# Optimization experiments

Measured on AMD Instinct MI355X. Metric: run time of the kernel, lower is better.

The kernel has to match this reference:

```python
import jax, jax.numpy as jnp
import numpy as np

B, S, D, E, H, K = 2, 2048, 1024, 8, 4096, 2  # batch, seq, n_embed, num_experts, 4*n_embed, top_k


def setup_inputs() -> dict:
    key = jax.random.key(0)
    ks = jax.random.split(key, 10)
    w = lambda k, shape: (jax.random.normal(k, shape, jnp.float32) * 0.02)
    return {
        "x": jax.random.normal(ks[0], (B, S, D), jnp.float32),
        "noise": jax.random.normal(ks[1], (B, S, E), jnp.float32),  # replaces torch.randn_like
        "Wr": w(ks[2], (D, E)),  # topkroute_linear
        "br": jnp.zeros((E,), jnp.float32),
        "Wn": w(ks[3], (D, E)),  # noise_linear
        "bn": jnp.zeros((E,), jnp.float32),
        "W1": w(ks[4], (E, D, H)),  # per-expert first Linear
        "b1": jnp.zeros((E, H), jnp.float32),
        "W2": w(ks[5], (E, H, D)),  # per-expert second Linear
        "b2": jnp.zeros((E, D), jnp.float32),
    }


def reference(x, noise, Wr, br, Wn, bn, W1, b1, W2, b2):
    # --- NoisyTopkRouter ---
    logits = jnp.einsum('bsd,de->bse', x, Wr) + br
    noise_logits = jnp.einsum('bsd,de->bse', x, Wn) + bn
    noisy_logits = logits + noise * jax.nn.softplus(noise_logits)
    _, topi = jax.lax.top_k(noisy_logits, K)                      # [B,S,K]
    sel = (topi[..., :, None] == jnp.arange(E)).any(axis=-2)      # [B,S,E] bool
    gates = jax.nn.softmax(jnp.where(sel, noisy_logits, -jnp.inf), axis=-1)  # sparse softmax
    softmax_gating = jax.nn.softmax(logits, axis=-1)

    # --- expert dispatch: gate is exactly 0 for non-selected experts, so the
    # masked gather/scatter loop equals a gate-weighted sum over all experts ---
    h = jax.nn.relu(jnp.einsum('bsd,edh->ebsh', x, W1) + b1[:, None, None, :])  # [E,B,S,H]
    y = jnp.einsum('ebsh,ehd->ebsd', h, W2) + b2[:, None, None, :]              # [E,B,S,D]
    final = jnp.einsum('bse,ebsd->bsd', gates, y)
    return final, softmax_gating
```

## Files before the change

kernel.cpp:

```cpp
#include <hip/hip_runtime.h>
#include <stdint.h>

#define T_TOK 4096
#define Dm    1024
#define Em    8
#define Hm    4096
#define NSLOT (2 * T_TOK)
#define KSPLIT 2

typedef __bf16 bf16x8 __attribute__((ext_vector_type(8)));
typedef float  f32x4  __attribute__((ext_vector_type(4)));
typedef unsigned short us8v __attribute__((ext_vector_type(8)));

__device__ __forceinline__ unsigned short f2bf(float f) {
  union { float f; unsigned int u; } c; c.f = f;
  unsigned int u = c.u;
  unsigned int r = u + 0x7fffu + ((u >> 16) & 1u);
  return (unsigned short)(r >> 16);
}

__device__ __forceinline__ void async16(const void* g, void* l) {
  __builtin_amdgcn_global_load_lds(
      (const __attribute__((address_space(1))) void*)g,
      (__attribute__((address_space(3))) void*)l, 16, 0, 0);
}

__global__ __launch_bounds__(256) void transpose_cvt_kernel(
    const float* __restrict__ src, unsigned short* __restrict__ dst, int R, int C) {
  __shared__ float tile[128][33];
  const int e = blockIdx.z;
  const float* s = src + (size_t)e * R * C;
  unsigned short* d = dst + (size_t)e * R * C;
  const int c0 = blockIdx.x * 32, r0 = blockIdx.y * 128;
  const int tid = threadIdx.x;

  const int lrow = tid >> 3, lc = (tid & 7) * 4;
#pragma unroll
  for (int p = 0; p < 4; ++p) {
    const int row = lrow + p * 32;
    float4 v = *(const float4*)(s + (size_t)(r0 + row) * C + c0 + lc);
    tile[row][lc + 0] = v.x; tile[row][lc + 1] = v.y;
    tile[row][lc + 2] = v.z; tile[row][lc + 3] = v.w;
  }
  __syncthreads();

  const int rb = (tid & 15) * 8;
#pragma unroll
  for (int p = 0; p < 2; ++p) {
    const int c = (tid >> 4) + p * 16;
    us8v o;
#pragma unroll
    for (int k = 0; k < 8; ++k) o[k] = f2bf(tile[rb + k][c]);
    *(us8v*)(d + (size_t)(c0 + c) * R + r0 + rb) = o;
  }
}

__global__ __launch_bounds__(256) void router_kernel(
    const float* __restrict__ x, const float* __restrict__ noise,
    const float* __restrict__ Wr, const float* __restrict__ br,
    const float* __restrict__ Wn, const float* __restrict__ bn,
    float* __restrict__ out_gating, int* __restrict__ lists,
    int* __restrict__ counts, float* __restrict__ gslot,
    unsigned short* __restrict__ xbf) {
  const int wave = threadIdx.x >> 6, lane = threadIdx.x & 63;
  const int t = blockIdx.x * 4 + wave;
  const float* xt = x + (size_t)t * Dm;
  float accR[Em] = {}, accN[Em] = {};
  for (int d = lane; d < Dm; d += 64) {
    const float xv = xt[d];
    xbf[(size_t)t * Dm + d] = f2bf(xv);
    const float* wr = Wr + d * Em;
    const float* wn = Wn + d * Em;
#pragma unroll
    for (int e = 0; e < Em; e++) { accR[e] += xv * wr[e]; accN[e] += xv * wn[e]; }
  }
#pragma unroll
  for (int e = 0; e < Em; e++)
    for (int off = 32; off > 0; off >>= 1) {
      accR[e] += __shfl_down(accR[e], off, 64);
      accN[e] += __shfl_down(accN[e], off, 64);
    }
  if (lane == 0) {
    float lg[Em], ny[Em];
#pragma unroll
    for (int e = 0; e < Em; e++) {
      lg[e] = accR[e] + br[e];
      float nl = accN[e] + bn[e];
      float sp = fmaxf(nl, 0.f) + log1pf(expf(-fabsf(nl)));
      ny[e] = lg[e] + noise[(size_t)t * Em + e] * sp;
    }
    int i0 = 0;
#pragma unroll
    for (int e = 1; e < Em; e++) if (ny[e] > ny[i0]) i0 = e;
    int i1 = (i0 == 0) ? 1 : 0;
#pragma unroll
    for (int e = 0; e < Em; e++) if (e != i0 && ny[e] > ny[i1]) i1 = e;
    const float e1 = expf(ny[i1] - ny[i0]);
    const float g0 = 1.f / (1.f + e1), g1 = e1 / (1.f + e1);
    float m = lg[0];
#pragma unroll
    for (int e = 1; e < Em; e++) m = fmaxf(m, lg[e]);
    float s = 0.f;
#pragma unroll
    for (int e = 0; e < Em; e++) s += expf(lg[e] - m);
#pragma unroll
    for (int e = 0; e < Em; e++) out_gating[(size_t)t * Em + e] = expf(lg[e] - m) / s;
    int p0 = atomicAdd(&counts[i0], 1); lists[i0 * T_TOK + p0] = t;
    int p1 = atomicAdd(&counts[i1], 1); lists[i1 * T_TOK + p1] = t;
    gslot[i0 * T_TOK + p0] = g0;
    gslot[i1 * T_TOK + p1] = g1;
  }
}

__global__ __launch_bounds__(256) void gemm1_kernel(
    const unsigned short* __restrict__ xbf, const unsigned short* __restrict__ w1bf,
    const float* __restrict__ b1, const int* __restrict__ counts,
    const int* __restrict__ lists, unsigned short* __restrict__ hbuf) {
  const int e = blockIdx.x;
  const int cnt = counts[e];
  const int m0 = blockIdx.y * 128;
  if (m0 >= cnt) return;
  const int n0 = blockIdx.z * 128;
  int base = 0;
  for (int i = 0; i < e; i++) base += counts[i];

  __shared__ __align__(16) unsigned short As[3][128 * 32];
  __shared__ __align__(16) unsigned short Bs[3][128 * 32];
  __shared__ int tok[128];

  const int tid = threadIdx.x;
  if (tid < 128) {
    int m = m0 + tid;
    tok[tid] = (m < cnt) ? lists[e * T_TOK + m] : 0;
  }
  __syncthreads();

  const int part = tid & 3;
  const int r0 = tid >> 2;
  const int r1 = r0 + 64;
  const size_t gA0 = (size_t)tok[r0] * Dm + part * 8;
  const size_t gA1 = (size_t)tok[r1] * Dm + part * 8;
  const size_t gB0 = ((size_t)e * Hm + n0 + r0) * Dm + part * 8;
  const size_t gB1 = ((size_t)e * Hm + n0 + r1) * Dm + part * 8;

  const int lane = tid & 63, wv = tid >> 6;
  const int quad = lane >> 4, l15 = lane & 15;
  const int wm = (wv >> 1) * 64, wn = (wv & 1) * 64;
  const int lds_off = wv * 512;

  f32x4 acc[4][4] = {};

  async16(xbf + gA0,       As[0] + lds_off);
  async16(xbf + gA1,       As[0] + 2048 + lds_off);
  async16(w1bf + gB0,      Bs[0] + lds_off);
  async16(w1bf + gB1,      Bs[0] + 2048 + lds_off);
  async16(xbf + gA0 + 32,  As[1] + lds_off);
  async16(xbf + gA1 + 32,  As[1] + 2048 + lds_off);
  async16(w1bf + gB0 + 32, Bs[1] + lds_off);
  async16(w1bf + gB1 + 32, Bs[1] + 2048 + lds_off);

  const int NI = Dm / 32;
  int cur = 0;
  for (int it = 0; it < NI; ++it) {
    if (it < NI - 1) {
      asm volatile("s_waitcnt vmcnt(4)" ::: "memory");
    } else {
      asm volatile("s_waitcnt vmcnt(0)" ::: "memory");
    }
    __builtin_amdgcn_s_barrier();
    __builtin_amdgcn_sched_barrier(0);
    if (it + 2 < NI) {
      const int k0 = (it + 2) * 32;
      int nb = cur + 2; if (nb >= 3) nb -= 3;
      async16(xbf + gA0 + k0, As[nb] + lds_off);
      async16(xbf + gA1 + k0, As[nb] + 2048 + lds_off);
      async16(w1bf + gB0 + k0, Bs[nb] + lds_off);
      async16(w1bf + gB1 + k0, Bs[nb] + 2048 + lds_off);
    }
    bf16x8 af[4], bfv[4];
#pragma unroll
    for (int i = 0; i < 4; i++)
      af[i] = *(const bf16x8*)(As[cur] + (wm + i * 16 + l15) * 32 + quad * 8);
#pragma unroll
    for (int j = 0; j < 4; j++)
      bfv[j] = *(const bf16x8*)(Bs[cur] + (wn + j * 16 + l15) * 32 + quad * 8);
#pragma unroll
    for (int i = 0; i < 4; i++)
#pragma unroll
      for (int j = 0; j < 4; j++)
        acc[i][j] = __builtin_amdgcn_mfma_f32_16x16x32_bf16(af[i], bfv[j], acc[i][j], 0, 0, 0);
    cur = (cur == 2) ? 0 : cur + 1;
  }

#pragma unroll
  for (int i = 0; i < 4; i++)
#pragma unroll
    for (int r = 0; r < 4; r++) {
      const int ml = wm + i * 16 + quad * 4 + r;
      const int m = m0 + ml;
      if (m < cnt) {
#pragma unroll
        for (int j = 0; j < 4; j++) {
          const int n = n0 + wn + j * 16 + l15;
          float v = acc[i][j][r] + b1[(size_t)e * Hm + n];
          v = fmaxf(v, 0.f);
          hbuf[(size_t)(base + m) * Hm + n] = f2bf(v);
        }
      }
    }
}

__global__ __launch_bounds__(256) void gemm2_kernel(
    const unsigned short* __restrict__ hbuf, const unsigned short* __restrict__ w2bf,
    const int* __restrict__ counts, const int* __restrict__ lists,
    const float* __restrict__ gslot, const float* __restrict__ b2,
    float* __restrict__ out) {
  const int e = blockIdx.x;
  const int ks = blockIdx.z & 1;
  const int cnt = counts[e];
  const int m0 = blockIdx.y * 128;
  if (m0 >= cnt) return;
  const int n0 = (blockIdx.z >> 1) * 128;
  int base = 0;
  for (int i = 0; i < e; i++) base += counts[i];
  const int kbase = ks * (Hm / KSPLIT);

  __shared__ __align__(16) unsigned short As[3][128 * 32];
  __shared__ __align__(16) unsigned short Bs[3][128 * 32];
  __shared__ int tok[128];
  __shared__ float gt[128];

  const int tid = threadIdx.x;
  if (tid < 128) {
    int m = m0 + tid;
    tok[tid] = (m < cnt) ? lists[e * T_TOK + m] : 0;
    gt[tid]  = (m < cnt) ? gslot[e * T_TOK + m] : 0.f;
  }
  __syncthreads();

  const int part = tid & 3;
  const int r0 = tid >> 2;
  const int r1 = r0 + 64;
  const int rowA0 = min(base + m0 + r0, NSLOT - 1);
  const int rowA1 = min(base + m0 + r1, NSLOT - 1);
  const size_t gA0 = (size_t)rowA0 * Hm + kbase + part * 8;
  const size_t gA1 = (size_t)rowA1 * Hm + kbase + part * 8;
  const size_t gB0 = ((size_t)e * Dm + n0 + r0) * Hm + kbase + part * 8;
  const size_t gB1 = ((size_t)e * Dm + n0 + r1) * Hm + kbase + part * 8;

  const int lane = tid & 63, wv = tid >> 6;
  const int quad = lane >> 4, l15 = lane & 15;
  const int wm = (wv >> 1) * 64, wn = (wv & 1) * 64;
  const int lds_off = wv * 512;

  f32x4 acc[4][4] = {};

  async16(hbuf + gA0,       As[0] + lds_off);
  async16(hbuf + gA1,       As[0] + 2048 + lds_off);
  async16(w2bf + gB0,       Bs[0] + lds_off);
  async16(w2bf + gB1,       Bs[0] + 2048 + lds_off);
  async16(hbuf + gA0 + 32,  As[1] + lds_off);
  async16(hbuf + gA1 + 32,  As[1] + 2048 + lds_off);
  async16(w2bf + gB0 + 32,  Bs[1] + lds_off);
  async16(w2bf + gB1 + 32,  Bs[1] + 2048 + lds_off);

  const int NI = Hm / KSPLIT / 32;
  int cur = 0;
  for (int it = 0; it < NI; ++it) {
    if (it < NI - 1) {
      asm volatile("s_waitcnt vmcnt(4)" ::: "memory");
    } else {
      asm volatile("s_waitcnt vmcnt(0)" ::: "memory");
    }
    __builtin_amdgcn_s_barrier();
    __builtin_amdgcn_sched_barrier(0);
    if (it + 2 < NI) {
      const int k0 = (it + 2) * 32;
      int nb = cur + 2; if (nb >= 3) nb -= 3;
      async16(hbuf + gA0 + k0, As[nb] + lds_off);
      async16(hbuf + gA1 + k0, As[nb] + 2048 + lds_off);
      async16(w2bf + gB0 + k0, Bs[nb] + lds_off);
      async16(w2bf + gB1 + k0, Bs[nb] + 2048 + lds_off);
    }
    bf16x8 af[4], bfv[4];
#pragma unroll
    for (int i = 0; i < 4; i++)
      af[i] = *(const bf16x8*)(As[cur] + (wm + i * 16 + l15) * 32 + quad * 8);
#pragma unroll
    for (int j = 0; j < 4; j++)
      bfv[j] = *(const bf16x8*)(Bs[cur] + (wn + j * 16 + l15) * 32 + quad * 8);
#pragma unroll
    for (int i = 0; i < 4; i++)
#pragma unroll
      for (int j = 0; j < 4; j++)
        acc[i][j] = __builtin_amdgcn_mfma_f32_16x16x32_bf16(af[i], bfv[j], acc[i][j], 0, 0, 0);
    cur = (cur == 2) ? 0 : cur + 1;
  }

#pragma unroll
  for (int i = 0; i < 4; i++)
#pragma unroll
    for (int r = 0; r < 4; r++) {
      const int ml = wm + i * 16 + quad * 4 + r;
      const int m = m0 + ml;
      if (m < cnt) {
        const int t = tok[ml];
        const float g = gt[ml];
        float* orow = out + (size_t)t * Dm + n0;
#pragma unroll
        for (int j = 0; j < 4; j++) {
          const int n = wn + j * 16 + l15;
          float v = acc[i][j][r];
          if (ks == 0) v += b2[(size_t)e * Dm + n0 + n];
          atomicAdd(orow + n, g * v);
        }
      }
    }
}

extern "C" void kernel_launch(void* const* d_in, const int* in_sizes, int n_in,
                              void* d_out, int out_size, void* d_ws, size_t ws_size,
                              hipStream_t stream) {
  const float* x     = (const float*)d_in[0];
  const float* noise = (const float*)d_in[1];
  const float* Wr    = (const float*)d_in[2];
  const float* br    = (const float*)d_in[3];
  const float* Wn    = (const float*)d_in[4];
  const float* bn    = (const float*)d_in[5];
  const float* W1    = (const float*)d_in[6];
  const float* b1    = (const float*)d_in[7];
  const float* W2    = (const float*)d_in[8];
  const float* b2    = (const float*)d_in[9];

  float* out        = (float*)d_out;
  float* out_gating = out + (size_t)T_TOK * Dm;

  char* ws = (char*)d_ws;
  unsigned short* w1bf = (unsigned short*)(ws);
  unsigned short* w2bf = (unsigned short*)(ws + 67108864);
  unsigned short* xbf  = (unsigned short*)(ws + 134217728);
  unsigned short* hbuf = (unsigned short*)(ws + 142606336);
  int*   lists         = (int*)(ws + 209715200);
  float* gslot         = (float*)(ws + 209846272);
  int*   counts        = (int*)(ws + 209977344);

  hipMemsetAsync(counts, 0, Em * sizeof(int), stream);
  hipMemsetAsync(out, 0, (size_t)T_TOK * Dm * sizeof(float), stream);

  transpose_cvt_kernel<<<dim3(Hm / 32, Dm / 128, Em), 256, 0, stream>>>(W1, w1bf, Dm, Hm);
  transpose_cvt_kernel<<<dim3(Dm / 32, Hm / 128, Em), 256, 0, stream>>>(W2, w2bf, Hm, Dm);

  router_kernel<<<T_TOK / 4, 256, 0, stream>>>(x, noise, Wr, br, Wn, bn,
                                               out_gating, lists, counts, gslot, xbf);

  gemm1_kernel<<<dim3(Em, 16, Hm / 128), 256, 0, stream>>>(xbf, w1bf, b1, counts, lists, hbuf);
  gemm2_kernel<<<dim3(Em, 16, (Dm / 128) * KSPLIT), 256, 0, stream>>>(hbuf, w2bf, counts, lists,
                                                                      gslot, b2, out);
}
```

Before: 753.9 us.

## Use 256x128 tiles with 512 threads and replace atomic scatter with combine kernel

```diff
diff --git a/kernel.cpp b/kernel.cpp
--- a/kernel.cpp
+++ b/kernel.cpp
@@ -6,7 +6,6 @@
 #define Em    8
 #define Hm    4096
 #define NSLOT (2 * T_TOK)
-#define KSPLIT 2
 
 typedef __bf16 bf16x8 __attribute__((ext_vector_type(8)));
 typedef float  f32x4  __attribute__((ext_vector_type(4)));
@@ -60,7 +59,8 @@
     const float* __restrict__ Wr, const float* __restrict__ br,
     const float* __restrict__ Wn, const float* __restrict__ bn,
     float* __restrict__ out_gating, int* __restrict__ lists,
-    int* __restrict__ counts, float* __restrict__ gslot,
+    int* __restrict__ counts, int* __restrict__ expt,
+    int* __restrict__ pos, float* __restrict__ gsel,
     unsigned short* __restrict__ xbf) {
   const int wave = threadIdx.x >> 6, lane = threadIdx.x & 63;
   const int t = blockIdx.x * 4 + wave;
@@ -107,41 +107,40 @@
     for (int e = 0; e < Em; e++) out_gating[(size_t)t * Em + e] = expf(lg[e] - m) / s;
     int p0 = atomicAdd(&counts[i0], 1); lists[i0 * T_TOK + p0] = t;
     int p1 = atomicAdd(&counts[i1], 1); lists[i1 * T_TOK + p1] = t;
-    gslot[i0 * T_TOK + p0] = g0;
-    gslot[i1 * T_TOK + p1] = g1;
-  }
-}
-
-__global__ __launch_bounds__(256) void gemm1_kernel(
+    expt[2 * t] = i0; expt[2 * t + 1] = i1;
+    pos[2 * t] = p0;  pos[2 * t + 1] = p1;
+    gsel[2 * t] = g0; gsel[2 * t + 1] = g1;
+  }
+}
+
+__global__ __launch_bounds__(512) void gemm1_kernel(
     const unsigned short* __restrict__ xbf, const unsigned short* __restrict__ w1bf,
     const float* __restrict__ b1, const int* __restrict__ counts,
     const int* __restrict__ lists, unsigned short* __restrict__ hbuf) {
   const int e = blockIdx.x;
   const int cnt = counts[e];
-  const int m0 = blockIdx.y * 128;
+  const int m0 = blockIdx.y * 256;
   if (m0 >= cnt) return;
   const int n0 = blockIdx.z * 128;
   int base = 0;
   for (int i = 0; i < e; i++) base += counts[i];
 
-  __shared__ __align__(16) unsigned short As[3][128 * 32];
+  __shared__ __align__(16) unsigned short As[3][256 * 32];
   __shared__ __align__(16) unsigned short Bs[3][128 * 32];
-  __shared__ int tok[128];
+  __shared__ int tok[256];
 
   const int tid = threadIdx.x;
-  if (tid < 128) {
+  if (tid < 256) {
     int m = m0 + tid;
     tok[tid] = (m < cnt) ? lists[e * T_TOK + m] : 0;
   }
   __syncthreads();
 
   const int part = tid & 3;
-  const int r0 = tid >> 2;
-  const int r1 = r0 + 64;
-  const size_t gA0 = (size_t)tok[r0] * Dm + part * 8;
-  const size_t gA1 = (size_t)tok[r1] * Dm + part * 8;
-  const size_t gB0 = ((size_t)e * Hm + n0 + r0) * Dm + part * 8;
-  const size_t gB1 = ((size_t)e * Hm + n0 + r1) * Dm + part * 8;
+  const int rr = tid >> 2;
+  const size_t gA0 = (size_t)tok[rr] * Dm + part * 8;
+  const size_t gA1 = (size_t)tok[rr + 128] * Dm + part * 8;
+  const size_t gB0 = ((size_t)e * Hm + n0 + rr) * Dm + part * 8;
 
   const int lane = tid & 63, wv = tid >> 6;
   const int quad = lane >> 4, l15 = lane & 15;
@@ -151,19 +150,17 @@
   f32x4 acc[4][4] = {};
 
   async16(xbf + gA0,       As[0] + lds_off);
-  async16(xbf + gA1,       As[0] + 2048 + lds_off);
+  async16(xbf + gA1,       As[0] + 4096 + lds_off);
   async16(w1bf + gB0,      Bs[0] + lds_off);
-  async16(w1bf + gB1,      Bs[0] + 2048 + lds_off);
   async16(xbf + gA0 + 32,  As[1] + lds_off);
-  async16(xbf + gA1 + 32,  As[1] + 2048 + lds_off);
+  async16(xbf + gA1 + 32,  As[1] + 4096 + lds_off);
   async16(w1bf + gB0 + 32, Bs[1] + lds_off);
-  async16(w1bf + gB1 + 32, Bs[1] + 2048 + lds_off);
 
   const int NI = Dm / 32;
   int cur = 0;
   for (int it = 0; it < NI; ++it) {
     if (it < NI - 1) {
-      asm volatile("s_waitcnt vmcnt(4)" ::: "memory");
+      asm volatile("s_waitcnt vmcnt(3)" ::: "memory");
     } else {
       asm volatile("s_waitcnt vmcnt(0)" ::: "memory");
     }
@@ -173,9 +170,8 @@
       const int k0 = (it + 2) * 32;
       int nb = cur + 2; if (nb >= 3) nb -= 3;
       async16(xbf + gA0 + k0, As[nb] + lds_off);
-      async16(xbf + gA1 + k0, As[nb] + 2048 + lds_off);
+      async16(xbf + gA1 + k0, As[nb] + 4096 + lds_off);
       async16(w1bf + gB0 + k0, Bs[nb] + lds_off);
-      async16(w1bf + gB1 + k0, Bs[nb] + 2048 + lds_off);
     }
     bf16x8 af[4], bfv[4];
 #pragma unroll
@@ -210,43 +206,28 @@
     }
 }
 
-__global__ __launch_bounds__(256) void gemm2_kernel(
+__global__ __launch_bounds__(512) void gemm2_kernel(
     const unsigned short* __restrict__ hbuf, const unsigned short* __restrict__ w2bf,
-    const int* __restrict__ counts, const int* __restrict__ lists,
-    const float* __restrict__ gslot, const float* __restrict__ b2,
-    float* __restrict__ out) {
+    const int* __restrict__ counts, float* __restrict__ ybuf) {
   const int e = blockIdx.x;
-  const int ks = blockIdx.z & 1;
   const int cnt = counts[e];
-  const int m0 = blockIdx.y * 128;
+  const int m0 = blockIdx.y * 256;
   if (m0 >= cnt) return;
-  const int n0 = (blockIdx.z >> 1) * 128;
+  const int n0 = blockIdx.z * 128;
   int base = 0;
   for (int i = 0; i < e; i++) base += counts[i];
-  const int kbase = ks * (Hm / KSPLIT);
-
-  __shared__ __align__(16) unsigned short As[3][128 * 32];
+
+  __shared__ __align__(16) unsigned short As[3][256 * 32];
   __shared__ __align__(16) unsigned short Bs[3][128 * 32];
-  __shared__ int tok[128];
-  __shared__ float gt[128];
 
   const int tid = threadIdx.x;
-  if (tid < 128) {
-    int m = m0 + tid;
-    tok[tid] = (m < cnt) ? lists[e * T_TOK + m] : 0;
-    gt[tid]  = (m < cnt) ? gslot[e * T_TOK + m] : 0.f;
-  }
-  __syncthreads();
-
   const int part = tid & 3;
-  const int r0 = tid >> 2;
-  const int r1 = r0 + 64;
-  const int rowA0 = min(base + m0 + r0, NSLOT - 1);
-  const int rowA1 = min(base + m0 + r1, NSLOT - 1);
-  const size_t gA0 = (size_t)rowA0 * Hm + kbase + part * 8;
-  const size_t gA1 = (size_t)rowA1 * Hm + kbase + part * 8;
-  const size_t gB0 = ((size_t)e * Dm + n0 + r0) * Hm + kbase + part * 8;
-  const size_t gB1 = ((size_t)e * Dm + n0 + r1) * Hm + kbase + part * 8;
+  const int rr = tid >> 2;
+  const int rowA0 = min(base + m0 + rr, NSLOT - 1);
+  const int rowA1 = min(base + m0 + rr + 128, NSLOT - 1);
+  const size_t gA0 = (size_t)rowA0 * Hm + part * 8;
+  const size_t gA1 = (size_t)rowA1 * Hm + part * 8;
+  const size_t gB0 = ((size_t)e * Dm + n0 + rr) * Hm + part * 8;
 
   const int lane = tid & 63, wv = tid >> 6;
   const int quad = lane >> 4, l15 = lane & 15;
@@ -256,19 +237,17 @@
   f32x4 acc[4][4] = {};
 
   async16(hbuf + gA0,       As[0] + lds_off);
-  async16(hbuf + gA1,       As[0] + 2048 + lds_off);
+  async16(hbuf + gA1,       As[0] + 4096 + lds_off);
   async16(w2bf + gB0,       Bs[0] + lds_off);
-  async16(w2bf + gB1,       Bs[0] + 2048 + lds_off);
   async16(hbuf + gA0 + 32,  As[1] + lds_off);
-  async16(hbuf + gA1 + 32,  As[1] + 2048 + lds_off);
+  async16(hbuf + gA1 + 32,  As[1] + 4096 + lds_off);
   async16(w2bf + gB0 + 32,  Bs[1] + lds_off);
-  async16(w2bf + gB1 + 32,  Bs[1] + 2048 + lds_off);
-
-  const int NI = Hm / KSPLIT / 32;
+
+  const int NI = Hm / 32;
   int cur = 0;
   for (int it = 0; it < NI; ++it) {
     if (it < NI - 1) {
-      asm volatile("s_waitcnt vmcnt(4)" ::: "memory");
+      asm volatile("s_waitcnt vmcnt(3)" ::: "memory");
     } else {
       asm volatile("s_waitcnt vmcnt(0)" ::: "memory");
     }
@@ -278,9 +257,8 @@
       const int k0 = (it + 2) * 32;
       int nb = cur + 2; if (nb >= 3) nb -= 3;
       async16(hbuf + gA0 + k0, As[nb] + lds_off);
-      async16(hbuf + gA1 + k0, As[nb] + 2048 + lds_off);
+      async16(hbuf + gA1 + k0, As[nb] + 4096 + lds_off);
       async16(w2bf + gB0 + k0, Bs[nb] + lds_off);
-      async16(w2bf + gB1 + k0, Bs[nb] + 2048 + lds_off);
     }
     bf16x8 af[4], bfv[4];
 #pragma unroll
@@ -304,18 +282,39 @@
       const int ml = wm + i * 16 + quad * 4 + r;
       const int m = m0 + ml;
       if (m < cnt) {
-        const int t = tok[ml];
-        const float g = gt[ml];
-        float* orow = out + (size_t)t * Dm + n0;
 #pragma unroll
         for (int j = 0; j < 4; j++) {
-          const int n = wn + j * 16 + l15;
-          float v = acc[i][j][r];
-          if (ks == 0) v += b2[(size_t)e * Dm + n0 + n];
-          atomicAdd(orow + n, g * v);
+          const int n = n0 + wn + j * 16 + l15;
+          ybuf[(size_t)(base + m) * Dm + n] = acc[i][j][r];
         }
       }
     }
+}
+
+__global__ __launch_bounds__(256) void combine_kernel(
+    const float* __restrict__ ybuf, const float* __restrict__ b2,
+    const int* __restrict__ counts, const int* __restrict__ expt,
+    const int* __restrict__ pos, const float* __restrict__ gsel,
+    float* __restrict__ out) {
+  const int t = blockIdx.x;
+  const int e0 = expt[2 * t], e1 = expt[2 * t + 1];
+  const float g0 = gsel[2 * t], g1 = gsel[2 * t + 1];
+  int b0 = 0, b1 = 0;
+  for (int i = 0; i < e0; i++) b0 += counts[i];
+  for (int i = 0; i < e1; i++) b1 += counts[i];
+  const size_t s0 = (size_t)(b0 + pos[2 * t]) * Dm;
+  const size_t s1 = (size_t)(b1 + pos[2 * t + 1]) * Dm;
+  const int c = threadIdx.x * 4;
+  float4 y0 = *(const float4*)(ybuf + s0 + c);
+  float4 y1 = *(const float4*)(ybuf + s1 + c);
+  float4 z0 = *(const float4*)(b2 + (size_t)e0 * Dm + c);
+  float4 z1 = *(const float4*)(b2 + (size_t)e1 * Dm + c);
+  float4 o;
+  o.x = g0 * (y0.x + z0.x) + g1 * (y1.x + z1.x);
+  o.y = g0 * (y0.y + z0.y) + g1 * (y1.y + z1.y);
+  o.z = g0 * (y0.z + z0.z) + g1 * (y1.z + z1.z);
+  o.w = g0 * (y0.w + z0.w) + g1 * (y1.w + z1.w);
+  *(float4*)(out + (size_t)t * Dm + c) = o;
 }
 
 extern "C" void kernel_launch(void* const* d_in, const int* in_sizes, int n_in,
@@ -340,20 +339,22 @@
   unsigned short* w2bf = (unsigned short*)(ws + 67108864);
   unsigned short* xbf  = (unsigned short*)(ws + 134217728);
   unsigned short* hbuf = (unsigned short*)(ws + 142606336);
+  float* ybuf          = (float*)(ws);
   int*   lists         = (int*)(ws + 209715200);
-  float* gslot         = (float*)(ws + 209846272);
-  int*   counts        = (int*)(ws + 209977344);
+  int*   expt          = (int*)(ws + 209846272);
+  int*   pos           = (int*)(ws + 209879040);
+  float* gsel          = (float*)(ws + 209911808);
+  int*   counts        = (int*)(ws + 209944576);
 
   hipMemsetAsync(counts, 0, Em * sizeof(int), stream);
-  hipMemsetAsync(out, 0, (size_t)T_TOK * Dm * sizeof(float), stream);
 
   transpose_cvt_kernel<<<dim3(Hm / 32, Dm / 128, Em), 256, 0, stream>>>(W1, w1bf, Dm, Hm);
   transpose_cvt_kernel<<<dim3(Dm / 32, Hm / 128, Em), 256, 0, stream>>>(W2, w2bf, Hm, Dm);
 
   router_kernel<<<T_TOK / 4, 256, 0, stream>>>(x, noise, Wr, br, Wn, bn,
-                                               out_gating, lists, counts, gslot, xbf);
-
-  gemm1_kernel<<<dim3(Em, 16, Hm / 128), 256, 0, stream>>>(xbf, w1bf, b1, counts, lists, hbuf);
-  gemm2_kernel<<<dim3(Em, 16, (Dm / 128) * KSPLIT), 256, 0, stream>>>(hbuf, w2bf, counts, lists,
-                                                                      gslot, b2, out);
-}
+                                               out_gating, lists, counts, expt, pos, gsel, xbf);
+
+  gemm1_kernel<<<dim3(Em, 8, Hm / 128), 512, 0, stream>>>(xbf, w1bf, b1, counts, lists, hbuf);
+  gemm2_kernel<<<dim3(Em, 8, Dm / 128), 512, 0, stream>>>(hbuf, w2bf, counts, ybuf);
+  combine_kernel<<<T_TOK, 256, 0, stream>>>(ybuf, b2, counts, expt, pos, gsel, out);
+}
```

New measurement: 735.7 us. 2.4% less time.
